# Performance work log

Hardware: AMD Instinct MI355X
Metric: run time of the kernel (lower is better)

The kernel has to match this reference:

```python
import jax, jax.numpy as jnp
import numpy as np

N = 50000      # total nodes (50 graphs x 1000 nodes)
G = 50         # number of graphs in the batch
NODE = 1000    # nodes per graph
E = 320000     # total edges (within-graph)
IN = 128
H1, H2 = 64, 128
HEADS = 4
NEG = 0.2      # LeakyReLU negative slope


def setup_inputs() -> dict:
    key = jax.random.key(0)
    ks = jax.random.split(key, 16)
    x = jax.random.normal(ks[0], (N, IN), jnp.float32)
    # edges confined to their own graph: per-graph offsets
    off = (jnp.arange(E) // (E // G)) * NODE
    src = jax.random.randint(ks[1], (E,), 0, NODE) + off
    dst = jax.random.randint(ks[2], (E,), 0, NODE) + off
    node2graph = jnp.arange(N) // NODE

    def lin(k, fan_in, fan_out):
        s = 1.0 / np.sqrt(fan_in)
        kw, kb = jax.random.split(k)
        return (jax.random.uniform(kw, (fan_in, fan_out), jnp.float32, -s, s),
                jax.random.uniform(kb, (fan_out,), jnp.float32, -s, s))

    W_src1, b_src1 = lin(ks[3], IN, HEADS * H1)
    W_dst1, b_dst1 = lin(ks[4], IN, HEADS * H1)
    attn1 = jax.random.normal(ks[5], (HEADS, H1), jnp.float32) * (1.0 / np.sqrt(H1))
    W_src2, b_src2 = lin(ks[6], H1, HEADS * H2)
    W_dst2, b_dst2 = lin(ks[7], H1, HEADS * H2)
    attn2 = jax.random.normal(ks[8], (HEADS, H2), jnp.float32) * (1.0 / np.sqrt(H2))
    gate_w, gate_b = lin(ks[9], H2, 1)
    return dict(x=x, src=src, dst=dst, node2graph=node2graph,
                W_src1=W_src1, b_src1=b_src1, W_dst1=W_dst1, b_dst1=b_dst1, attn1=attn1,
                W_src2=W_src2, b_src2=b_src2, W_dst2=W_dst2, b_dst2=b_dst2, attn2=attn2,
                gate_w=gate_w, gate_b=gate_b)


def gatv2_layer(h, src, dst, W_src, b_src, W_dst, b_dst, attn):
    # DGL GATv2Conv: e_ij = a^T LeakyReLU(W_src h_j + W_dst h_i), edge softmax over dst
    H, D = attn.shape
    fs = (h @ W_src + b_src).reshape(-1, H, D)  # [N,H,D]
    fd = (h @ W_dst + b_dst).reshape(-1, H, D)
    e = jax.nn.leaky_relu(fs[src] + fd[dst], NEG)        # [E,H,D]
    logits = jnp.einsum('ehd,hd->eh', e, attn)           # [E,H]
    m = jax.ops.segment_max(logits, dst, num_segments=h.shape[0])
    ex = jnp.exp(logits - m[dst])
    denom = jax.ops.segment_sum(ex, dst, num_segments=h.shape[0])
    alpha = ex / denom[dst]                              # [E,H]
    out = jax.ops.segment_sum(alpha[:, :, None] * fs[src], dst,
                              num_segments=h.shape[0])   # [N,H,D]
    return out


def reference(x, src, dst, node2graph,
              W_src1, b_src1, W_dst1, b_dst1, attn1,
              W_src2, b_src2, W_dst2, b_dst2, attn2,
              gate_w, gate_b):
    # layer 1 + head-wise maxpool -> [N, H1]
    h = gatv2_layer(x, src, dst, W_src1, b_src1, W_dst1, b_dst1, attn1).max(axis=1)
    # layer 2 + head-wise maxpool -> [N, H2]
    h = gatv2_layer(h, src, dst, W_src2, b_src2, W_dst2, b_dst2, attn2).max(axis=1)
    # global attention pooling: softmax(gate) over nodes per graph, weighted sum
    gate = h @ gate_w + gate_b                           # [N,1]
    gm = jax.ops.segment_max(gate, node2graph, num_segments=G)
    ge = jnp.exp(gate - gm[node2graph])
    gs = jax.ops.segment_sum(ge, node2graph, num_segments=G)
    alpha = ge / gs[node2graph]                          # [N,1]
    return jax.ops.segment_sum(alpha * h, node2graph, num_segments=G)  # [G, H2]
```

## Files before the change

kernel.cpp:

```cpp
#include <hip/hip_runtime.h>
#include <math.h>

#define NN 50000
#define GG 50
#define NODE 1000
#define EE 320000
#define HEADS 4

typedef __attribute__((ext_vector_type(8))) short short8;
typedef __attribute__((ext_vector_type(8))) __bf16 bf16x8;
typedef __attribute__((ext_vector_type(4))) float f32x4;

__device__ __forceinline__ unsigned short f2bf(float f) {
    unsigned int u = __float_as_uint(f);
    u = (u + 0x7fffu + ((u >> 16) & 1u)) >> 16;
    return (unsigned short)u;
}
__device__ __forceinline__ float bf2f(unsigned short s) {
    return __uint_as_float(((unsigned int)s) << 16);
}

__global__ void cvt_f32_bf16(const float* __restrict__ in, unsigned short* __restrict__ outp, int n4) {
    int i = blockIdx.x * 256 + threadIdx.x;
    if (i < n4) {
        float4 f = *(const float4*)(in + (size_t)i * 4);
        ushort4 o;
        o.x = f2bf(f.x); o.y = f2bf(f.y); o.z = f2bf(f.z); o.w = f2bf(f.w);
        *(ushort4*)(outp + (size_t)i * 4) = o;
    }
}

__global__ void wt_cvt(const float* __restrict__ W, unsigned short* __restrict__ Wt, int K, int N_) {
    int i = blockIdx.x * 256 + threadIdx.x;
    if (i < K * N_) {
        int n = i / K, k = i - n * K;
        Wt[i] = f2bf(W[(size_t)k * N_ + n]);
    }
}

__global__ void count_deg(const int* __restrict__ dst, int* __restrict__ deg, int E_) {
    int i = blockIdx.x * 256 + threadIdx.x;
    if (i < E_) atomicAdd(&deg[dst[i]], 1);
}

__global__ void scan1(const int* __restrict__ deg, int* __restrict__ bsum, int Nn) {
    __shared__ int sh[256];
    int i = blockIdx.x * 256 + threadIdx.x;
    sh[threadIdx.x] = (i < Nn) ? deg[i] : 0;
    __syncthreads();
    for (int s = 128; s > 0; s >>= 1) {
        if (threadIdx.x < s) sh[threadIdx.x] += sh[threadIdx.x + s];
        __syncthreads();
    }
    if (threadIdx.x == 0) bsum[blockIdx.x] = sh[0];
}

__global__ void scan2(int* __restrict__ bsum, int nb, int* __restrict__ rowptr, int Nn, int E_) {
    if (threadIdx.x == 0 && blockIdx.x == 0) {
        int acc = 0;
        for (int i = 0; i < nb; ++i) { int v = bsum[i]; bsum[i] = acc; acc += v; }
        rowptr[Nn] = E_;
    }
}

__global__ void scan3(const int* __restrict__ deg, const int* __restrict__ bsum,
                      int* __restrict__ rowptr, int* __restrict__ cursor, int Nn) {
    __shared__ int sh[256];
    int i = blockIdx.x * 256 + threadIdx.x;
    int v = (i < Nn) ? deg[i] : 0;
    sh[threadIdx.x] = v;
    __syncthreads();
    for (int s = 1; s < 256; s <<= 1) {
        int t = (threadIdx.x >= s) ? sh[threadIdx.x - s] : 0;
        __syncthreads();
        sh[threadIdx.x] += t;
        __syncthreads();
    }
    if (i < Nn) {
        int ex = sh[threadIdx.x] - v + bsum[blockIdx.x];
        rowptr[i] = ex;
        cursor[i] = ex;
    }
}

__global__ void scatter_edges(const int* __restrict__ src, const int* __restrict__ dst,
                              int* __restrict__ cursor, int* __restrict__ csrc, int E_) {
    int i = blockIdx.x * 256 + threadIdx.x;
    if (i < E_) { int pos = atomicAdd(&cursor[dst[i]], 1); csrc[pos] = src[i]; }
}

template<int K>
__global__ __launch_bounds__(256)
void gemm_mfma(const unsigned short* __restrict__ A, const unsigned short* __restrict__ Wt,
               const float* __restrict__ bias, unsigned short* __restrict__ C,
               int M, int Ncols) {
    __shared__ short A_lds[128 * K];
    __shared__ short B_lds[128 * K];
    constexpr int CH = K / 8;
    constexpr int ROWB = K * 2;
    int tid = threadIdx.x;
    int lane = tid & 63, wave = tid >> 6;
    int row0 = blockIdx.y * 128, col0 = blockIdx.x * 128;

    for (int c = tid; c < 128 * CH; c += 256) {
        int r = c / CH, kc = c - r * CH;
        int gr = row0 + r; if (gr >= M) gr = M - 1;
        short8 v = *(const short8*)(A + (size_t)gr * K + kc * 8);
        *(short8*)((char*)A_lds + r * ROWB + ((kc * 16) ^ ((r & 7) << 4))) = v;
    }
    for (int c = tid; c < 128 * CH; c += 256) {
        int r = c / CH, kc = c - r * CH;
        short8 v = *(const short8*)(Wt + (size_t)(col0 + r) * K + kc * 8);
        *(short8*)((char*)B_lds + r * ROWB + ((kc * 16) ^ ((r & 7) << 4))) = v;
    }
    __syncthreads();

    int wr = wave >> 1, wc = wave & 1;
    f32x4 acc[4][4] = {};
    #pragma unroll
    for (int ks = 0; ks < K / 32; ++ks) {
        int kbyte = ks * 64 + ((lane >> 4) << 4);
        short8 a[4], b[4];
        #pragma unroll
        for (int m = 0; m < 4; ++m) {
            int r = wr * 64 + m * 16 + (lane & 15);
            a[m] = *(const short8*)((const char*)A_lds + r * ROWB + (kbyte ^ ((r & 7) << 4)));
        }
        #pragma unroll
        for (int n = 0; n < 4; ++n) {
            int r = wc * 64 + n * 16 + (lane & 15);
            b[n] = *(const short8*)((const char*)B_lds + r * ROWB + (kbyte ^ ((r & 7) << 4)));
        }
        #pragma unroll
        for (int m = 0; m < 4; ++m)
            #pragma unroll
            for (int n = 0; n < 4; ++n)
                acc[m][n] = __builtin_amdgcn_mfma_f32_16x16x32_bf16(
                    __builtin_bit_cast(bf16x8, a[m]), __builtin_bit_cast(bf16x8, b[n]),
                    acc[m][n], 0, 0, 0);
    }

    #pragma unroll
    for (int m = 0; m < 4; ++m) {
        int grb = row0 + wr * 64 + m * 16 + ((lane >> 4) << 2);
        #pragma unroll
        for (int q = 0; q < 4; ++q) {
            int gr = grb + q;
            if (gr < M) {
                #pragma unroll
                for (int n = 0; n < 4; ++n) {
                    int gc = col0 + wc * 64 + n * 16 + (lane & 15);
                    C[(size_t)gr * Ncols + gc] = f2bf(acc[m][n][q] + bias[gc]);
                }
            }
        }
    }
}

template<int D>
__global__ void gat_fused(const int* __restrict__ rowptr, const int* __restrict__ csrc,
                          const unsigned short* __restrict__ fs, const unsigned short* __restrict__ fd,
                          const float* __restrict__ attn, void* __restrict__ hout, int Nn) {
    int lane = threadIdx.x & 63;
    int wave = (blockIdx.x * blockDim.x + threadIdx.x) >> 6;
    int nw = (gridDim.x * blockDim.x) >> 6;
    constexpr int VE = D / 16;
    constexpr int HD = HEADS * D;
    int head = lane >> 4;
    int doff = (lane & 15) * VE;

    float at[VE];
    #pragma unroll
    for (int j = 0; j < VE; ++j) at[j] = attn[head * D + doff + j];

    for (int n = wave; n < Nn; n += nw) {
        int b = rowptr[n], e_ = rowptr[n + 1];
        float r[VE];
        if (b == e_) {
            #pragma unroll
            for (int k = 0; k < VE; ++k) r[k] = 0.f;
        } else {
            float fdf[VE];
            if constexpr (VE == 4) {
                ushort4 vd = *(const ushort4*)(fd + (size_t)n * HD + lane * 4);
                fdf[0] = bf2f(vd.x); fdf[1] = bf2f(vd.y); fdf[2] = bf2f(vd.z); fdf[3] = bf2f(vd.w);
            } else {
                short8 vd = *(const short8*)(fd + (size_t)n * HD + lane * 8);
                #pragma unroll
                for (int k = 0; k < 8; ++k) fdf[k] = bf2f((unsigned short)vd[k]);
            }
            float m = -INFINITY, l = 0.f;
            float acc[VE];
            #pragma unroll
            for (int k = 0; k < VE; ++k) acc[k] = 0.f;

            for (int j = b; j < e_; ++j) {
                int s = csrc[j];
                float fsf[VE];
                if constexpr (VE == 4) {
                    ushort4 vs = *(const ushort4*)(fs + (size_t)s * HD + lane * 4);
                    fsf[0] = bf2f(vs.x); fsf[1] = bf2f(vs.y); fsf[2] = bf2f(vs.z); fsf[3] = bf2f(vs.w);
                } else {
                    short8 vs = *(const short8*)(fs + (size_t)s * HD + lane * 8);
                    #pragma unroll
                    for (int k = 0; k < 8; ++k) fsf[k] = bf2f((unsigned short)vs[k]);
                }
                float p = 0.f;
                #pragma unroll
                for (int k = 0; k < VE; ++k) {
                    float v = fsf[k] + fdf[k];
                    v = v >= 0.f ? v : 0.2f * v;
                    p += v * at[k];
                }
                p += __shfl_xor(p, 1);
                p += __shfl_xor(p, 2);
                p += __shfl_xor(p, 4);
                p += __shfl_xor(p, 8);
                float mn = fmaxf(m, p);
                float sc = __expf(m - mn);
                float pw = __expf(p - mn);
                l = l * sc + pw;
                #pragma unroll
                for (int k = 0; k < VE; ++k) acc[k] = acc[k] * sc + pw * fsf[k];
                m = mn;
            }
            float inv = 1.f / l;
            #pragma unroll
            for (int k = 0; k < VE; ++k) r[k] = acc[k] * inv;
        }
        #pragma unroll
        for (int k = 0; k < VE; ++k) {
            r[k] = fmaxf(r[k], __shfl_xor(r[k], 16));
            r[k] = fmaxf(r[k], __shfl_xor(r[k], 32));
        }
        if (lane < 16) {
            if constexpr (VE == 4) {
                ushort4 o;
                o.x = f2bf(r[0]); o.y = f2bf(r[1]); o.z = f2bf(r[2]); o.w = f2bf(r[3]);
                *(ushort4*)((unsigned short*)hout + (size_t)n * 64 + doff) = o;
            } else {
                float* hp = (float*)hout + (size_t)n * 128 + doff;
                *(float4*)hp = make_float4(r[0], r[1], r[2], r[3]);
                *(float4*)(hp + 4) = make_float4(r[4], r[5], r[6], r[7]);
            }
        }
    }
}

__global__ void pool_kernel(const float* __restrict__ h2, const float* __restrict__ gate_w,
                            const float* __restrict__ gate_b, float* __restrict__ out) {
    __shared__ float gate[NODE];
    __shared__ float red[256];
    int g = blockIdx.x;
    int tid = threadIdx.x;
    const float* hb = h2 + (size_t)g * NODE * 128;
    float gb = gate_b[0];
    for (int n = tid; n < NODE; n += 256) {
        const float* r = hb + (size_t)n * 128;
        float acc = 0.f;
        #pragma unroll 8
        for (int k = 0; k < 128; ++k) acc += r[k] * gate_w[k];
        gate[n] = acc + gb;
    }
    __syncthreads();
    float m = -INFINITY;
    for (int n = tid; n < NODE; n += 256) m = fmaxf(m, gate[n]);
    red[tid] = m;
    __syncthreads();
    for (int s = 128; s > 0; s >>= 1) {
        if (tid < s) red[tid] = fmaxf(red[tid], red[tid + s]);
        __syncthreads();
    }
    m = red[0];
    __syncthreads();
    float ssum = 0.f;
    for (int n = tid; n < NODE; n += 256) {
        float e = __expf(gate[n] - m);
        gate[n] = e;
        ssum += e;
    }
    red[tid] = ssum;
    __syncthreads();
    for (int s = 128; s > 0; s >>= 1) {
        if (tid < s) red[tid] += red[tid + s];
        __syncthreads();
    }
    float inv = 1.f / red[0];
    __syncthreads();
    if (tid < 128) {
        float acc = 0.f;
        for (int n = 0; n < NODE; ++n) acc += gate[n] * hb[(size_t)n * 128 + tid];
        out[g * 128 + tid] = acc * inv;
    }
}

extern "C" void kernel_launch(void* const* d_in, const int* in_sizes, int n_in,
                              void* d_out, int out_size, void* d_ws, size_t ws_size,
                              hipStream_t stream) {
    const float* x      = (const float*)d_in[0];
    const int*   src    = (const int*)d_in[1];
    const int*   dst    = (const int*)d_in[2];
    const float* W_src1 = (const float*)d_in[4];
    const float* b_src1 = (const float*)d_in[5];
    const float* W_dst1 = (const float*)d_in[6];
    const float* b_dst1 = (const float*)d_in[7];
    const float* attn1  = (const float*)d_in[8];
    const float* W_src2 = (const float*)d_in[9];
    const float* b_src2 = (const float*)d_in[10];
    const float* W_dst2 = (const float*)d_in[11];
    const float* b_dst2 = (const float*)d_in[12];
    const float* attn2  = (const float*)d_in[13];
    const float* gate_w = (const float*)d_in[14];
    const float* gate_b = (const float*)d_in[15];
    float* out = (float*)d_out;

    char* p = (char*)d_ws;
    auto alloc = [&](size_t bytes) -> void* {
        void* r = (void*)p;
        p += (bytes + 255) & ~(size_t)255;
        return r;
    };
    unsigned short* fs     = (unsigned short*)alloc((size_t)NN * 512 * 2);
    unsigned short* fd     = (unsigned short*)alloc((size_t)NN * 512 * 2);
    unsigned short* h1     = (unsigned short*)alloc((size_t)NN * 64 * 2);
    float*          h2     = (float*)alloc((size_t)NN * 128 * 4);
    unsigned short* x_bf   = (unsigned short*)alloc((size_t)NN * 128 * 2);
    unsigned short* Wt1s   = (unsigned short*)alloc((size_t)128 * 256 * 2);
    unsigned short* Wt1d   = (unsigned short*)alloc((size_t)128 * 256 * 2);
    unsigned short* Wt2s   = (unsigned short*)alloc((size_t)64 * 512 * 2);
    unsigned short* Wt2d   = (unsigned short*)alloc((size_t)64 * 512 * 2);
    int*            deg    = (int*)alloc((size_t)NN * 4);
    int*            rowptr = (int*)alloc((size_t)(NN + 1) * 4);
    int*            cursor = (int*)alloc((size_t)NN * 4);
    int*            csrc   = (int*)alloc((size_t)EE * 4);
    int*            bsum   = (int*)alloc(4096);

    cvt_f32_bf16<<<(NN * 128 / 4 + 255) / 256, 256, 0, stream>>>(x, x_bf, NN * 128 / 4);
    wt_cvt<<<(128 * 256 + 255) / 256, 256, 0, stream>>>(W_src1, Wt1s, 128, 256);
    wt_cvt<<<(128 * 256 + 255) / 256, 256, 0, stream>>>(W_dst1, Wt1d, 128, 256);
    wt_cvt<<<(64 * 512 + 255) / 256, 256, 0, stream>>>(W_src2, Wt2s, 64, 512);
    wt_cvt<<<(64 * 512 + 255) / 256, 256, 0, stream>>>(W_dst2, Wt2d, 64, 512);

    hipMemsetAsync(deg, 0, (size_t)NN * 4, stream);
    count_deg<<<(EE + 255) / 256, 256, 0, stream>>>(dst, deg, EE);
    int nb = (NN + 255) / 256;
    scan1<<<nb, 256, 0, stream>>>(deg, bsum, NN);
    scan2<<<1, 64, 0, stream>>>(bsum, nb, rowptr, NN, EE);
    scan3<<<nb, 256, 0, stream>>>(deg, bsum, rowptr, cursor, NN);
    scatter_edges<<<(EE + 255) / 256, 256, 0, stream>>>(src, dst, cursor, csrc, EE);

    int rowtiles = (NN + 127) / 128;

    gemm_mfma<128><<<dim3(2, rowtiles), 256, 0, stream>>>(x_bf, Wt1s, b_src1, fs, NN, 256);
    gemm_mfma<128><<<dim3(2, rowtiles), 256, 0, stream>>>(x_bf, Wt1d, b_dst1, fd, NN, 256);
    gat_fused<64><<<2048, 256, 0, stream>>>(rowptr, csrc, fs, fd, attn1, h1, NN);

    gemm_mfma<64><<<dim3(4, rowtiles), 256, 0, stream>>>(h1, Wt2s, b_src2, fs, NN, 512);
    gemm_mfma<64><<<dim3(4, rowtiles), 256, 0, stream>>>(h1, Wt2d, b_dst2, fd, NN, 512);
    gat_fused<128><<<2048, 256, 0, stream>>>(rowptr, csrc, fs, fd, attn2, h2, NN);

    pool_kernel<<<GG, 256, 0, stream>>>(h2, gate_w, gate_b, out);
}
```

Measured before the change: 397.2 us.

## Prefetch next neighbor features, use lazy softmax rescaling, and contiguous node ranges

The GAT aggregation kernel now software-prefetches the next source node's feature row while computing on the current one, which hides the latency of the dependent gather. The online softmax only rescales the accumulator when some lane's logit exceeds the running max by more than a threshold, skipping two exps and the rescale multiplies on most edges. Each wave now processes a contiguous block of nodes with a swizzled block index instead of striding across the grid, improving locality within a graph. The lazy-rescale threshold lets exp arguments reach up to about e^8, which is numerically safe in fp32. The uneven contiguous split may cause some load imbalance across waves.

```diff
diff --git a/kernel.cpp b/kernel.cpp
--- a/kernel.cpp
+++ b/kernel.cpp
@@ -158,22 +158,29 @@
 }
 
 template<int D>
-__global__ void gat_fused(const int* __restrict__ rowptr, const int* __restrict__ csrc,
-                          const unsigned short* __restrict__ fs, const unsigned short* __restrict__ fd,
-                          const float* __restrict__ attn, void* __restrict__ hout, int Nn) {
-    int lane = threadIdx.x & 63;
-    int wave = (blockIdx.x * blockDim.x + threadIdx.x) >> 6;
-    int nw = (gridDim.x * blockDim.x) >> 6;
+__global__ __launch_bounds__(256)
+void gat_fused(const int* __restrict__ rowptr, const int* __restrict__ csrc,
+               const unsigned short* __restrict__ fs, const unsigned short* __restrict__ fd,
+               const float* __restrict__ attn, void* __restrict__ hout, int Nn) {
     constexpr int VE = D / 16;
     constexpr int HD = HEADS * D;
+    int lane = threadIdx.x & 63;
     int head = lane >> 4;
     int doff = (lane & 15) * VE;
+
+    int bid = blockIdx.x;
+    int sb = (bid & 7) * (gridDim.x >> 3) + (bid >> 3);
+    int wid = sb * 4 + (threadIdx.x >> 6);
+    int nwaves = gridDim.x * 4;
+    int per = (Nn + nwaves - 1) / nwaves;
+    int n0 = wid * per;
+    int n1 = min(n0 + per, Nn);
 
     float at[VE];
     #pragma unroll
     for (int j = 0; j < VE; ++j) at[j] = attn[head * D + doff + j];
 
-    for (int n = wave; n < Nn; n += nw) {
+    for (int n = n0; n < n1; ++n) {
         int b = rowptr[n], e_ = rowptr[n + 1];
         float r[VE];
         if (b == e_) {
@@ -194,16 +201,25 @@
             #pragma unroll
             for (int k = 0; k < VE; ++k) acc[k] = 0.f;
 
+            ushort4 buf4;
+            short8  buf8;
+            {
+                int s0 = csrc[b];
+                if constexpr (VE == 4) buf4 = *(const ushort4*)(fs + (size_t)s0 * HD + lane * 4);
+                else                   buf8 = *(const short8*)(fs + (size_t)s0 * HD + lane * 8);
+            }
             for (int j = b; j < e_; ++j) {
-                int s = csrc[j];
                 float fsf[VE];
                 if constexpr (VE == 4) {
-                    ushort4 vs = *(const ushort4*)(fs + (size_t)s * HD + lane * 4);
-                    fsf[0] = bf2f(vs.x); fsf[1] = bf2f(vs.y); fsf[2] = bf2f(vs.z); fsf[3] = bf2f(vs.w);
+                    fsf[0] = bf2f(buf4.x); fsf[1] = bf2f(buf4.y); fsf[2] = bf2f(buf4.z); fsf[3] = bf2f(buf4.w);
                 } else {
-                    short8 vs = *(const short8*)(fs + (size_t)s * HD + lane * 8);
                     #pragma unroll
-                    for (int k = 0; k < 8; ++k) fsf[k] = bf2f((unsigned short)vs[k]);
+                    for (int k = 0; k < 8; ++k) fsf[k] = bf2f((unsigned short)buf8[k]);
+                }
+                if (j + 1 < e_) {
+                    int sn = csrc[j + 1];
+                    if constexpr (VE == 4) buf4 = *(const ushort4*)(fs + (size_t)sn * HD + lane * 4);
+                    else                   buf8 = *(const short8*)(fs + (size_t)sn * HD + lane * 8);
                 }
                 float p = 0.f;
                 #pragma unroll
@@ -216,13 +232,18 @@
                 p += __shfl_xor(p, 2);
                 p += __shfl_xor(p, 4);
                 p += __shfl_xor(p, 8);
-                float mn = fmaxf(m, p);
-                float sc = __expf(m - mn);
-                float pw = __expf(p - mn);
-                l = l * sc + pw;
+                if (__any(p > m + 8.f)) {
+                    float mn = fmaxf(m, p);
+                    float sc = __expf(m - mn);
+                    l *= sc;
+                    #pragma unroll
+                    for (int k = 0; k < VE; ++k) acc[k] *= sc;
+                    m = mn;
+                }
+                float pw = __expf(p - m);
+                l += pw;
                 #pragma unroll
-                for (int k = 0; k < VE; ++k) acc[k] = acc[k] * sc + pw * fsf[k];
-                m = mn;
+                for (int k = 0; k < VE; ++k) acc[k] += pw * fsf[k];
             }
             float inv = 1.f / l;
             #pragma unroll
```

Result: no change. 400.3 us (+0.8%).

## Unroll GAT edge loop by two with register prefetch and lazy softmax rescale

Applied to the files above, without the earlier changes.

Restructures the per-node edge loop in the fused GATv2 attention kernel to process two edges per iteration. The feature rows for the next pair of edges are prefetched into registers, so gather latency can overlap with the current compute. The online-softmax running max is now only rescaled when a new logit exceeds the current max by more than a threshold (wave-uniform via __any), which removes most exp and rescale work per edge. This adds register pressure, a launch bound of 256 is added to guide allocation, and the deferred max allows exponents up to e^8 before rescaling.

```diff
diff --git a/kernel.cpp b/kernel.cpp
--- a/kernel.cpp
+++ b/kernel.cpp
@@ -158,14 +158,15 @@
 }
 
 template<int D>
-__global__ void gat_fused(const int* __restrict__ rowptr, const int* __restrict__ csrc,
-                          const unsigned short* __restrict__ fs, const unsigned short* __restrict__ fd,
-                          const float* __restrict__ attn, void* __restrict__ hout, int Nn) {
+__global__ __launch_bounds__(256)
+void gat_fused(const int* __restrict__ rowptr, const int* __restrict__ csrc,
+               const unsigned short* __restrict__ fs, const unsigned short* __restrict__ fd,
+               const float* __restrict__ attn, void* __restrict__ hout, int Nn) {
+    constexpr int VE = D / 16;
+    constexpr int HD = HEADS * D;
     int lane = threadIdx.x & 63;
     int wave = (blockIdx.x * blockDim.x + threadIdx.x) >> 6;
     int nw = (gridDim.x * blockDim.x) >> 6;
-    constexpr int VE = D / 16;
-    constexpr int HD = HEADS * D;
     int head = lane >> 4;
     int doff = (lane & 15) * VE;
 
@@ -194,35 +195,73 @@
             #pragma unroll
             for (int k = 0; k < VE; ++k) acc[k] = 0.f;
 
-            for (int j = b; j < e_; ++j) {
-                int s = csrc[j];
-                float fsf[VE];
+            ushort4 c40 = {}, c41 = {}, p40 = {}, p41 = {};
+            short8  c80 = {}, c81 = {}, p80 = {}, p81 = {};
+            if constexpr (VE == 4) {
+                c40 = *(const ushort4*)(fs + (size_t)csrc[b] * HD + lane * 4);
+                if (b + 1 < e_) c41 = *(const ushort4*)(fs + (size_t)csrc[b + 1] * HD + lane * 4);
+            } else {
+                c80 = *(const short8*)(fs + (size_t)csrc[b] * HD + lane * 8);
+                if (b + 1 < e_) c81 = *(const short8*)(fs + (size_t)csrc[b + 1] * HD + lane * 8);
+            }
+
+            for (int j = b; j < e_; j += 2) {
+                bool two = (j + 1 < e_);
+                if (j + 2 < e_) {
+                    int sn = csrc[j + 2];
+                    if constexpr (VE == 4) p40 = *(const ushort4*)(fs + (size_t)sn * HD + lane * 4);
+                    else                   p80 = *(const short8*)(fs + (size_t)sn * HD + lane * 8);
+                }
+                if (j + 3 < e_) {
+                    int sn = csrc[j + 3];
+                    if constexpr (VE == 4) p41 = *(const ushort4*)(fs + (size_t)sn * HD + lane * 4);
+                    else                   p81 = *(const short8*)(fs + (size_t)sn * HD + lane * 8);
+                }
+                float fs0[VE], fs1[VE];
                 if constexpr (VE == 4) {
-                    ushort4 vs = *(const ushort4*)(fs + (size_t)s * HD + lane * 4);
-                    fsf[0] = bf2f(vs.x); fsf[1] = bf2f(vs.y); fsf[2] = bf2f(vs.z); fsf[3] = bf2f(vs.w);
+                    fs0[0] = bf2f(c40.x); fs0[1] = bf2f(c40.y); fs0[2] = bf2f(c40.z); fs0[3] = bf2f(c40.w);
+                    fs1[0] = bf2f(c41.x); fs1[1] = bf2f(c41.y); fs1[2] = bf2f(c41.z); fs1[3] = bf2f(c41.w);
                 } else {
-                    short8 vs = *(const short8*)(fs + (size_t)s * HD + lane * 8);
                     #pragma unroll
-                    for (int k = 0; k < 8; ++k) fsf[k] = bf2f((unsigned short)vs[k]);
-                }
-                float p = 0.f;
+                    for (int k = 0; k < 8; ++k) fs0[k] = bf2f((unsigned short)c80[k]);
+                    #pragma unroll
+                    for (int k = 0; k < 8; ++k) fs1[k] = bf2f((unsigned short)c81[k]);
+                }
+                float p0 = 0.f, p1 = 0.f;
                 #pragma unroll
                 for (int k = 0; k < VE; ++k) {
-                    float v = fsf[k] + fdf[k];
-                    v = v >= 0.f ? v : 0.2f * v;
-                    p += v * at[k];
-                }
-                p += __shfl_xor(p, 1);
-                p += __shfl_xor(p, 2);
-                p += __shfl_xor(p, 4);
-                p += __shfl_xor(p, 8);
-                float mn = fmaxf(m, p);
-                float sc = __expf(m - mn);
-                float pw = __expf(p - mn);
-                l = l * sc + pw;
+                    float v0 = fs0[k] + fdf[k];
+                    v0 = v0 >= 0.f ? v0 : 0.2f * v0;
+                    p0 += v0 * at[k];
+                    float v1 = fs1[k] + fdf[k];
+                    v1 = v1 >= 0.f ? v1 : 0.2f * v1;
+                    p1 += v1 * at[k];
+                }
+                p0 += __shfl_xor(p0, 1); p1 += __shfl_xor(p1, 1);
+                p0 += __shfl_xor(p0, 2); p1 += __shfl_xor(p1, 2);
+                p0 += __shfl_xor(p0, 4); p1 += __shfl_xor(p1, 4);
+                p0 += __shfl_xor(p0, 8); p1 += __shfl_xor(p1, 8);
+                float pm = two ? fmaxf(p0, p1) : p0;
+                if (__any(pm > m + 8.f)) {
+                    float mn = fmaxf(m, pm);
+                    float sc = __expf(m - mn);
+                    l *= sc;
+                    #pragma unroll
+                    for (int k = 0; k < VE; ++k) acc[k] *= sc;
+                    m = mn;
+                }
+                float w0 = __expf(p0 - m);
+                l += w0;
                 #pragma unroll
-                for (int k = 0; k < VE; ++k) acc[k] = acc[k] * sc + pw * fsf[k];
-                m = mn;
+                for (int k = 0; k < VE; ++k) acc[k] += w0 * fs0[k];
+                if (two) {
+                    float w1 = __expf(p1 - m);
+                    l += w1;
+                    #pragma unroll
+                    for (int k = 0; k < VE; ++k) acc[k] += w1 * fs1[k];
+                }
+                if constexpr (VE == 4) { c40 = p40; c41 = p41; }
+                else                   { c80 = p80; c81 = p81; }
             }
             float inv = 1.f / l;
             #pragma unroll
```

Result: no change. 402.4 us (+1.3%).
